# Optimization experiments

Measured on AMD Instinct MI355X. Metric: run time of the kernel, lower is better.

The kernel has to match this reference:

```python
import jax, jax.numpy as jnp
import numpy as np

LATENT_SIZE = 1024
WORD_SIZE = 64
NB_WORD = 8192
COMMIT_VQ = 2.5
BATCH = 2048


def setup_inputs() -> dict:
    key = jax.random.key(0)
    k1, k2, k3 = jax.random.split(key, 3)
    z_mean = jax.random.normal(k1, (BATCH, LATENT_SIZE), dtype=jnp.float32)
    z_log_var = jax.random.normal(k2, (BATCH, LATENT_SIZE), dtype=jnp.float32)
    # Embedding initialized uniform(-1/nb_word, 1/nb_word) in the torch module;
    # use normal here for a numerically non-degenerate correctness baseline.
    emb_weight = jax.random.normal(k3, (NB_WORD, WORD_SIZE), dtype=jnp.float32)
    return {"z_mean": z_mean, "z_log_var": z_log_var, "emb_weight": emb_weight}


def reference(z_mean, z_log_var, emb_weight):
    sg = jax.lax.stop_gradient
    input_shape = z_mean.shape
    # (B * latent/word, word)
    z = z_mean.reshape(-1, LATENT_SIZE // WORD_SIZE, WORD_SIZE)
    z_flat = z.reshape(-1, WORD_SIZE)
    # squared euclidean distances: (N, nb_word)
    distances = (
        jnp.sum(z_flat ** 2, axis=1, keepdims=True)
        + jnp.sum(emb_weight ** 2, axis=1)
        - 2.0 * jnp.einsum("bd,nd->bn", z_flat, emb_weight)
    )
    min_idx = jnp.argmin(distances, axis=1)  # (N,)
    z_q = emb_weight[min_idx].reshape(z.shape)  # gather codebook vectors
    loss = (
        jnp.mean((sg(z_q) - z) ** 2)
        + COMMIT_VQ * jnp.mean((z_q - sg(z)) ** 2)
    )
    z_q_st = z + sg(z_q - z)  # straight-through estimator
    return z_q_st.reshape(input_shape), loss
```

## Files before the change

### kernel.cpp

```cpp
#include <hip/hip_runtime.h>
#include <math.h>

#define LATENT   1024
#define WORD     64
#define NB_WORD  8192
#define BATCH    2048
#define NROWS    (BATCH * LATENT / WORD)
#define NELEM    (BATCH * LATENT)

#define NCHUNK   8
#define CWCHUNK  (NB_WORD / NCHUNK)
#define TPC      (CWCHUNK / 16)
#define NTILE    (NB_WORD / 16)
#define PKTS     (NTILE * 6 * 64)

typedef __attribute__((ext_vector_type(8))) __bf16 bf16x8;
typedef __attribute__((ext_vector_type(4))) float  f32x4;

__global__ __launch_bounds__(256) void vq_prep_kernel(
    const float* __restrict__ emb, float* __restrict__ e2,
    bf16x8* __restrict__ epack) {
    int m = blockIdx.x * 256 + threadIdx.x;
    int tile = m >> 4, l15 = m & 15;
    float s0 = 0.f, s1 = 0.f, s2 = 0.f, s3 = 0.f;
#pragma unroll
    for (int Ks = 0; Ks < 2; ++Ks) {
#pragma unroll
        for (int q = 0; q < 4; ++q) {
            const float4* s4 = reinterpret_cast<const float4*>(
                emb + (size_t)m * WORD + Ks * 32 + q * 8);
            float4 a = s4[0], b = s4[1];
            float tv[8] = {a.x, a.y, a.z, a.w, b.x, b.y, b.z, b.w};
            bf16x8 oh, om, ol;
#pragma unroll
            for (int e = 0; e < 8; ++e) {
                float v = tv[e];
                if ((e & 3) == 0) s0 = fmaf(v, v, s0);
                else if ((e & 3) == 1) s1 = fmaf(v, v, s1);
                else if ((e & 3) == 2) s2 = fmaf(v, v, s2);
                else s3 = fmaf(v, v, s3);
                __bf16 h  = (__bf16)v;
                float r1  = v - (float)h;
                __bf16 mm = (__bf16)r1;
                float r2  = r1 - (float)mm;
                __bf16 lo = (__bf16)r2;
                oh[e] = h; om[e] = mm; ol[e] = lo;
            }
            size_t base = ((size_t)tile * 6) * 64 + q * 16 + l15;
            epack[base + (size_t)(0 * 2 + Ks) * 64] = oh;
            epack[base + (size_t)(1 * 2 + Ks) * 64] = om;
            epack[base + (size_t)(2 * 2 + Ks) * 64] = ol;
        }
    }
    e2[m] = (s0 + s1) + (s2 + s3);
}

#define MFMA16 __builtin_amdgcn_mfma_f32_16x16x32_bf16

__global__ __launch_bounds__(256)
__attribute__((amdgpu_waves_per_eu(4, 8)))
void vq_argmin_kernel(
    const float* __restrict__ z, const bf16x8* __restrict__ epack,
    const float* __restrict__ e2, unsigned long long* __restrict__ best) {

    const int tid   = threadIdx.x;
    const int lane  = tid & 63;
    const int wband = tid >> 6;
    const int l15   = lane & 15;
    const int l4    = lane >> 4;
    const int rowbase   = blockIdx.x * 128 + wband * 32;
    const int tile0     = blockIdx.y * TPC;
    const int chunkbase = blockIdx.y * CWCHUNK;
    const float* e2g    = e2 + chunkbase;
    const int off       = (blockIdx.x & 15) * 4;

    bf16x8 A[2][2][3];
    const float4* zf4 = reinterpret_cast<const float4*>(z);
#pragma unroll
    for (int mt = 0; mt < 2; ++mt) {
        int row = rowbase + mt * 16 + l15;
#pragma unroll
        for (int Ks = 0; Ks < 2; ++Ks) {
            float4 v0 = zf4[(size_t)row * 16 + Ks * 8 + l4 * 2];
            float4 v1 = zf4[(size_t)row * 16 + Ks * 8 + l4 * 2 + 1];
            float tv[8] = {v0.x, v0.y, v0.z, v0.w, v1.x, v1.y, v1.z, v1.w};
#pragma unroll
            for (int e = 0; e < 8; ++e) {
                float v = tv[e];
                __bf16 h  = (__bf16)v;
                float r1  = v - (float)h;
                __bf16 m  = (__bf16)r1;
                float r2  = r1 - (float)m;
                __bf16 lo = (__bf16)r2;
                A[mt][Ks][0][e] = h;
                A[mt][Ks][1][e] = m;
                A[mt][Ks][2][e] = lo;
            }
        }
    }

    float bestd[8] = {INFINITY, INFINITY, INFINITY, INFINITY,
                      INFINITY, INFINITY, INFINITY, INFINITY};
    int   bt[8]    = {0, 0, 0, 0, 0, 0, 0, 0};

    bf16x8 Ph0, Pm0, Pl0, Ph1, Pm1, Pl1;
    bf16x8 Qh0, Qm0, Ql0, Qh1, Qm1, Ql1;
    float  e2p, e2q;

#define STAGE(S, E2V, TN)                                                   \
    {                                                                       \
        const bf16x8* ep_ = epack + (size_t)(tile0 + (TN)) * 384;           \
        S##h0 = ep_[lane];        S##h1 = ep_[64 + lane];                   \
        S##m0 = ep_[128 + lane];  S##m1 = ep_[192 + lane];                  \
        S##l0 = ep_[256 + lane];  S##l1 = ep_[320 + lane];                  \
        E2V   = e2g[(TN) * 16 + l15];                                       \
    }

#define PHASE(S, E2V, TCUR)                                                 \
    {                                                                       \
        f32x4 acc0 = {0.f, 0.f, 0.f, 0.f};                                  \
        f32x4 acc1 = {0.f, 0.f, 0.f, 0.f};                                  \
        acc0 = MFMA16(A[0][0][0], S##h0, acc0, 0, 0, 0);                    \
        acc1 = MFMA16(A[1][0][0], S##h0, acc1, 0, 0, 0);                    \
        acc0 = MFMA16(A[0][0][1], S##h0, acc0, 0, 0, 0);                    \
        acc1 = MFMA16(A[1][0][1], S##h0, acc1, 0, 0, 0);                    \
        acc0 = MFMA16(A[0][0][2], S##h0, acc0, 0, 0, 0);                    \
        acc1 = MFMA16(A[1][0][2], S##h0, acc1, 0, 0, 0);                    \
        acc0 = MFMA16(A[0][0][1], S##m0, acc0, 0, 0, 0);                    \
        acc1 = MFMA16(A[1][0][1], S##m0, acc1, 0, 0, 0);                    \
        acc0 = MFMA16(A[0][0][0], S##m0, acc0, 0, 0, 0);                    \
        acc1 = MFMA16(A[1][0][0], S##m0, acc1, 0, 0, 0);                    \
        acc0 = MFMA16(A[0][0][0], S##l0, acc0, 0, 0, 0);                    \
        acc1 = MFMA16(A[1][0][0], S##l0, acc1, 0, 0, 0);                    \
        acc0 = MFMA16(A[0][1][0], S##h1, acc0, 0, 0, 0);                    \
        acc1 = MFMA16(A[1][1][0], S##h1, acc1, 0, 0, 0);                    \
        acc0 = MFMA16(A[0][1][1], S##h1, acc0, 0, 0, 0);                    \
        acc1 = MFMA16(A[1][1][1], S##h1, acc1, 0, 0, 0);                    \
        acc0 = MFMA16(A[0][1][2], S##h1, acc0, 0, 0, 0);                    \
        acc1 = MFMA16(A[1][1][2], S##h1, acc1, 0, 0, 0);                    \
        acc0 = MFMA16(A[0][1][1], S##m1, acc0, 0, 0, 0);                    \
        acc1 = MFMA16(A[1][1][1], S##m1, acc1, 0, 0, 0);                    \
        acc0 = MFMA16(A[0][1][0], S##m1, acc0, 0, 0, 0);                    \
        acc1 = MFMA16(A[1][1][0], S##m1, acc1, 0, 0, 0);                    \
        acc0 = MFMA16(A[0][1][0], S##l1, acc0, 0, 0, 0);                    \
        acc1 = MFMA16(A[1][1][0], S##l1, acc1, 0, 0, 0);                    \
        _Pragma("unroll")                                                   \
        for (int v = 0; v < 4; ++v) {                                       \
            float d0 = fmaf(-2.0f, acc0[v], E2V);                           \
            if (d0 < bestd[v])     { bestd[v]     = d0; bt[v]     = TCUR; } \
            float d1 = fmaf(-2.0f, acc1[v], E2V);                           \
            if (d1 < bestd[4 + v]) { bestd[4 + v] = d1; bt[4 + v] = TCUR; } \
        }                                                                   \
    }

    STAGE(P, e2p, off);

    for (int tt = 0; tt < TPC; tt += 2) {
        const int tA = (tt + off) & (TPC - 1);
        const int tB = (tt + 1 + off) & (TPC - 1);
        const int tC = (tt + 2 + off) & (TPC - 1);

        STAGE(Q, e2q, tB);
        PHASE(P, e2p, tA);
        STAGE(P, e2p, tC);
        PHASE(Q, e2q, tB);
    }
#undef STAGE
#undef PHASE

#pragma unroll
    for (int mt = 0; mt < 2; ++mt) {
#pragma unroll
        for (int v = 0; v < 4; ++v) {
            float bd = bestd[mt * 4 + v];
            int   cw = chunkbase + bt[mt * 4 + v] * 16 + l15;
            unsigned db = __float_as_uint(bd);
            db = (db & 0x80000000u) ? ~db : (db | 0x80000000u);
            unsigned long long key =
                ((unsigned long long)db << 32) | (unsigned)cw;
#pragma unroll
            for (int off2 = 1; off2 < 16; off2 <<= 1) {
                unsigned long long o = __shfl_xor(key, off2);
                key = (o < key) ? o : key;
            }
            if (l15 == 0)
                atomicMin(&best[rowbase + mt * 16 + l4 * 4 + v], key);
        }
    }
}

__global__ __launch_bounds__(256) void vq_out_kernel(
    const float* __restrict__ z, const float* __restrict__ emb,
    const unsigned long long* __restrict__ best,
    float* __restrict__ out, float* __restrict__ lsum) {
    const int base = (blockIdx.x * 256 + threadIdx.x) * 8;
    const int row  = base >> 6;
    const int m    = (int)(best[row] & 0xFFFFFFFFull);

    const float4* zp = reinterpret_cast<const float4*>(z + base);
    const float4* qp = reinterpret_cast<const float4*>(emb + (size_t)m * WORD + (base & 63));
    float4* op = reinterpret_cast<float4*>(out + base);

    float s = 0.f;
#pragma unroll
    for (int i = 0; i < 2; ++i) {
        float4 zv = zp[i];
        float4 qv = qp[i];
        float dx = qv.x - zv.x, dy = qv.y - zv.y, dz = qv.z - zv.z, dw = qv.w - zv.w;
        float4 ov;
        ov.x = zv.x + dx; ov.y = zv.y + dy; ov.z = zv.z + dz; ov.w = zv.w + dw;
        op[i] = ov;
        s += dx*dx + dy*dy + dz*dz + dw*dw;
    }

#pragma unroll
    for (int off = 32; off > 0; off >>= 1) s += __shfl_down(s, off);
    __shared__ float wsum[4];
    int lane = threadIdx.x & 63, wid = threadIdx.x >> 6;
    if (lane == 0) wsum[wid] = s;
    __syncthreads();
    if (threadIdx.x == 0)
        atomicAdd(lsum, (wsum[0] + wsum[1]) + (wsum[2] + wsum[3]));
}

__global__ void vq_loss_kernel(const float* __restrict__ lsum,
                               float* __restrict__ loss_out) {
    float mean = lsum[0] * (1.0f / (float)NELEM);
    loss_out[0] = mean + 2.5f * mean;
}

extern "C" void kernel_launch(void* const* d_in, const int* in_sizes, int n_in,
                              void* d_out, int out_size, void* d_ws, size_t ws_size,
                              hipStream_t stream) {
    const float* z   = (const float*)d_in[0];
    const float* emb = (const float*)d_in[2];
    float* out = (float*)d_out;

    bf16x8* epack = (bf16x8*)d_ws;
    float*  e2    = (float*)((char*)d_ws + (size_t)PKTS * 16);
    unsigned long long* best =
        (unsigned long long*)((char*)e2 + NB_WORD * sizeof(float));
    float* lsum = (float*)((char*)best + NROWS * sizeof(unsigned long long));

    hipMemsetAsync(best, 0xFF, NROWS * sizeof(unsigned long long), stream);
    hipMemsetAsync(lsum, 0, sizeof(float), stream);

    vq_prep_kernel<<<NB_WORD / 256, 256, 0, stream>>>(emb, e2, epack);
    vq_argmin_kernel<<<dim3(NROWS / 128, NCHUNK), 256, 0, stream>>>(
        z, epack, e2, best);
    vq_out_kernel<<<NELEM / (256 * 8), 256, 0, stream>>>(z, emb, best, out, lsum);
    vq_loss_kernel<<<1, 1, 0, stream>>>(lsum, out + NELEM);
}
```

Before: 203.6 us.

## Stream codebook tiles via async global-to-LDS loads with double buffering

Replaces register-staged codebook loads with global_load_lds direct-to-LDS transfers into a per-wave double buffer, waiting on vmcnt before reading the current tile from LDS. It also splits the MFMA chain into four independent accumulators (one per K half) to shorten dependency chains, and pins waves_per_eu to 4. The aim is to free VGPRs and overlap memory with MFMA. It adds 48KB LDS per block and an LDS read hop, and relies on the hand-written vmcnt count being right.

```diff
diff --git a/kernel.cpp b/kernel.cpp
--- a/kernel.cpp
+++ b/kernel.cpp
@@ -55,13 +55,21 @@
     e2[m] = (s0 + s1) + (s2 + s3);
 }
 
+__device__ __forceinline__ void gload_lds16(const char* g, char* l) {
+    __builtin_amdgcn_global_load_lds(
+        (const __attribute__((address_space(1))) void*)g,
+        (__attribute__((address_space(3))) void*)l, 16, 0, 0);
+}
+
 #define MFMA16 __builtin_amdgcn_mfma_f32_16x16x32_bf16
 
 __global__ __launch_bounds__(256)
-__attribute__((amdgpu_waves_per_eu(4, 8)))
+__attribute__((amdgpu_waves_per_eu(4, 4)))
 void vq_argmin_kernel(
     const float* __restrict__ z, const bf16x8* __restrict__ epack,
     const float* __restrict__ e2, unsigned long long* __restrict__ best) {
+
+    __shared__ __align__(16) char le[4][2][6144];
 
     const int tid   = threadIdx.x;
     const int lane  = tid & 63;
@@ -99,73 +107,85 @@
         }
     }
 
+    char* lbase = &le[wband][0][0];
+
+    {
+        const char* src = (const char*)epack + (size_t)(tile0 + off) * 6144 + lane * 16;
+#pragma unroll
+        for (int j = 0; j < 6; ++j)
+            gload_lds16(src + j * 1024, lbase + j * 1024);
+    }
+    float e2A = e2g[off * 16 + l15];
+    float e2B;
+
     float bestd[8] = {INFINITY, INFINITY, INFINITY, INFINITY,
                       INFINITY, INFINITY, INFINITY, INFINITY};
     int   bt[8]    = {0, 0, 0, 0, 0, 0, 0, 0};
 
-    bf16x8 Ph0, Pm0, Pl0, Ph1, Pm1, Pl1;
-    bf16x8 Qh0, Qm0, Ql0, Qh1, Qm1, Ql1;
-    float  e2p, e2q;
-
-#define STAGE(S, E2V, TN)                                                   \
+#define PHASE(BUFOFF, E2CUR, E2NXT, TCUR, TNXT)                             \
     {                                                                       \
-        const bf16x8* ep_ = epack + (size_t)(tile0 + (TN)) * 384;           \
-        S##h0 = ep_[lane];        S##h1 = ep_[64 + lane];                   \
-        S##m0 = ep_[128 + lane];  S##m1 = ep_[192 + lane];                  \
-        S##l0 = ep_[256 + lane];  S##l1 = ep_[320 + lane];                  \
-        E2V   = e2g[(TN) * 16 + l15];                                       \
-    }
-
-#define PHASE(S, E2V, TCUR)                                                 \
-    {                                                                       \
-        f32x4 acc0 = {0.f, 0.f, 0.f, 0.f};                                  \
-        f32x4 acc1 = {0.f, 0.f, 0.f, 0.f};                                  \
-        acc0 = MFMA16(A[0][0][0], S##h0, acc0, 0, 0, 0);                    \
-        acc1 = MFMA16(A[1][0][0], S##h0, acc1, 0, 0, 0);                    \
-        acc0 = MFMA16(A[0][0][1], S##h0, acc0, 0, 0, 0);                    \
-        acc1 = MFMA16(A[1][0][1], S##h0, acc1, 0, 0, 0);                    \
-        acc0 = MFMA16(A[0][0][2], S##h0, acc0, 0, 0, 0);                    \
-        acc1 = MFMA16(A[1][0][2], S##h0, acc1, 0, 0, 0);                    \
-        acc0 = MFMA16(A[0][0][1], S##m0, acc0, 0, 0, 0);                    \
-        acc1 = MFMA16(A[1][0][1], S##m0, acc1, 0, 0, 0);                    \
-        acc0 = MFMA16(A[0][0][0], S##m0, acc0, 0, 0, 0);                    \
-        acc1 = MFMA16(A[1][0][0], S##m0, acc1, 0, 0, 0);                    \
-        acc0 = MFMA16(A[0][0][0], S##l0, acc0, 0, 0, 0);                    \
-        acc1 = MFMA16(A[1][0][0], S##l0, acc1, 0, 0, 0);                    \
-        acc0 = MFMA16(A[0][1][0], S##h1, acc0, 0, 0, 0);                    \
-        acc1 = MFMA16(A[1][1][0], S##h1, acc1, 0, 0, 0);                    \
-        acc0 = MFMA16(A[0][1][1], S##h1, acc0, 0, 0, 0);                    \
-        acc1 = MFMA16(A[1][1][1], S##h1, acc1, 0, 0, 0);                    \
-        acc0 = MFMA16(A[0][1][2], S##h1, acc0, 0, 0, 0);                    \
-        acc1 = MFMA16(A[1][1][2], S##h1, acc1, 0, 0, 0);                    \
-        acc0 = MFMA16(A[0][1][1], S##m1, acc0, 0, 0, 0);                    \
-        acc1 = MFMA16(A[1][1][1], S##m1, acc1, 0, 0, 0);                    \
-        acc0 = MFMA16(A[0][1][0], S##m1, acc0, 0, 0, 0);                    \
-        acc1 = MFMA16(A[1][1][0], S##m1, acc1, 0, 0, 0);                    \
-        acc0 = MFMA16(A[0][1][0], S##l1, acc0, 0, 0, 0);                    \
-        acc1 = MFMA16(A[1][1][0], S##l1, acc1, 0, 0, 0);                    \
+        const char* srcn = (const char*)epack +                             \
+                           (size_t)(tile0 + (TNXT)) * 6144 + lane * 16;     \
+        char* dstn = lbase + ((BUFOFF) ^ 6144);                             \
+        _Pragma("unroll")                                                   \
+        for (int j = 0; j < 6; ++j)                                         \
+            gload_lds16(srcn + j * 1024, dstn + j * 1024);                  \
+        E2NXT = e2g[(TNXT) * 16 + l15];                                     \
+        asm volatile("s_waitcnt vmcnt(7)" ::: "memory");                    \
+        asm volatile("" :: "v"(E2CUR));         \
+        const char* bb = lbase + (BUFOFF) + lane * 16;                      \
+        bf16x8 Bh0 = *reinterpret_cast<const bf16x8*>(bb);                  \
+        bf16x8 Bh1 = *reinterpret_cast<const bf16x8*>(bb + 1024);           \
+        bf16x8 Bm0 = *reinterpret_cast<const bf16x8*>(bb + 2048);           \
+        bf16x8 Bm1 = *reinterpret_cast<const bf16x8*>(bb + 3072);           \
+        bf16x8 Bl0 = *reinterpret_cast<const bf16x8*>(bb + 4096);           \
+        bf16x8 Bl1 = *reinterpret_cast<const bf16x8*>(bb + 5120);           \
+        f32x4 a00 = {0.f, 0.f, 0.f, 0.f};                                   \
+        f32x4 a01 = {0.f, 0.f, 0.f, 0.f};                                   \
+        f32x4 a10 = {0.f, 0.f, 0.f, 0.f};                                   \
+        f32x4 a11 = {0.f, 0.f, 0.f, 0.f};                                   \
+          \
+        a00 = MFMA16(A[0][0][0], Bh0, a00, 0, 0, 0);                        \
+        a10 = MFMA16(A[1][0][0], Bh0, a10, 0, 0, 0);                        \
+        a01 = MFMA16(A[0][1][0], Bh1, a01, 0, 0, 0);                        \
+        a11 = MFMA16(A[1][1][0], Bh1, a11, 0, 0, 0);                        \
+        a00 = MFMA16(A[0][0][1], Bh0, a00, 0, 0, 0);                        \
+        a10 = MFMA16(A[1][0][1], Bh0, a10, 0, 0, 0);                        \
+        a01 = MFMA16(A[0][1][1], Bh1, a01, 0, 0, 0);                        \
+        a11 = MFMA16(A[1][1][1], Bh1, a11, 0, 0, 0);                        \
+        a00 = MFMA16(A[0][0][2], Bh0, a00, 0, 0, 0);                        \
+        a10 = MFMA16(A[1][0][2], Bh0, a10, 0, 0, 0);                        \
+        a01 = MFMA16(A[0][1][2], Bh1, a01, 0, 0, 0);                        \
+        a11 = MFMA16(A[1][1][2], Bh1, a11, 0, 0, 0);                        \
+        a00 = MFMA16(A[0][0][1], Bm0, a00, 0, 0, 0);                        \
+        a10 = MFMA16(A[1][0][1], Bm0, a10, 0, 0, 0);                        \
+        a01 = MFMA16(A[0][1][1], Bm1, a01, 0, 0, 0);                        \
+        a11 = MFMA16(A[1][1][1], Bm1, a11, 0, 0, 0);                        \
+        a00 = MFMA16(A[0][0][0], Bm0, a00, 0, 0, 0);                        \
+        a10 = MFMA16(A[1][0][0], Bm0, a10, 0, 0, 0);                        \
+        a01 = MFMA16(A[0][1][0], Bm1, a01, 0, 0, 0);                        \
+        a11 = MFMA16(A[1][1][0], Bm1, a11, 0, 0, 0);                        \
+        a00 = MFMA16(A[0][0][0], Bl0, a00, 0, 0, 0);                        \
+        a10 = MFMA16(A[1][0][0], Bl0, a10, 0, 0, 0);                        \
+        a01 = MFMA16(A[0][1][0], Bl1, a01, 0, 0, 0);                        \
+        a11 = MFMA16(A[1][1][0], Bl1, a11, 0, 0, 0);                        \
         _Pragma("unroll")                                                   \
         for (int v = 0; v < 4; ++v) {                                       \
-            float d0 = fmaf(-2.0f, acc0[v], E2V);                           \
-            if (d0 < bestd[v])     { bestd[v]     = d0; bt[v]     = TCUR; } \
-            float d1 = fmaf(-2.0f, acc1[v], E2V);                           \
-            if (d1 < bestd[4 + v]) { bestd[4 + v] = d1; bt[4 + v] = TCUR; } \
+            float d0 = fmaf(-2.0f, a00[v] + a01[v], E2CUR);                 \
+            if (d0 < bestd[v])     { bestd[v]     = d0; bt[v]     = (TCUR); } \
+            float d1 = fmaf(-2.0f, a10[v] + a11[v], E2CUR);                 \
+            if (d1 < bestd[4 + v]) { bestd[4 + v] = d1; bt[4 + v] = (TCUR); } \
         }                                                                   \
     }
 
-    STAGE(P, e2p, off);
-
+    int t0 = off;
     for (int tt = 0; tt < TPC; tt += 2) {
-        const int tA = (tt + off) & (TPC - 1);
-        const int tB = (tt + 1 + off) & (TPC - 1);
-        const int tC = (tt + 2 + off) & (TPC - 1);
-
-        STAGE(Q, e2q, tB);
-        PHASE(P, e2p, tA);
-        STAGE(P, e2p, tC);
-        PHASE(Q, e2q, tB);
-    }
-#undef STAGE
+        int t1 = t0 + 1; if (t1 >= TPC) t1 -= TPC;
+        int t2 = t1 + 1; if (t2 >= TPC) t2 -= TPC;
+        PHASE(0,    e2A, e2B, t0, t1);
+        PHASE(6144, e2B, e2A, t1, t2);
+        t0 = t2;
+    }
 #undef PHASE
 
 #pragma unroll
```

After: 222.3 us. 1.09x slower.
